# Kernel optimization log

Hardware: AMD Instinct MI355X
Metric: run time of the kernel (lower is better)

The kernel has to match this reference:

```python
import jax, jax.numpy as jnp
import numpy as np

N, D = 16384, 2048

def setup_inputs() -> dict:
    key = jax.random.key(0)
    k1, k2 = jax.random.split(key)
    F = jax.random.normal(k1, (N, D), dtype=jnp.float32)
    F_star = jax.random.normal(k2, (N, D), dtype=jnp.float32)
    lambda_r = jnp.float32(1.0)
    return {"F": F, "F_star": F_star, "lambda_r": lambda_r}

def reference(F, F_star, lambda_r):
    # trace(F F^T Fs Fs^T) == ||F^T Fs||_F^2 (cyclic trace property);
    # avoids materializing the n x n Gram matrices the torch code forms.
    G = jnp.einsum('nd,ne->de', F, F_star)  # [D, D]
    return lambda_r * jnp.sum(G * G)
```

## Files before the change

kernel.cpp:

```cpp
#include <hip/hip_runtime.h>
#include <hip/hip_bf16.h>

#define N_ROWS 16384
#define D_DIM  2048
#define SPLITK 4
#define NS     (N_ROWS / 32)
#define NP     (D_DIM / 128)


typedef __attribute__((ext_vector_type(8))) short short8;
typedef __attribute__((ext_vector_type(4))) float f32x4;
typedef __attribute__((ext_vector_type(8))) unsigned short ushort8;
typedef __attribute__((ext_vector_type(4))) unsigned short ushort4v;

#define GPTR(p) ((const __attribute__((address_space(1))) void*)(p))
#define LPTR(p) ((__attribute__((address_space(3))) void*)(p))

__device__ __forceinline__ unsigned short f2bf(float x) {
  __hip_bfloat16 b = __float2bfloat16(x);
  return *reinterpret_cast<unsigned short*>(&b);
}
__device__ __forceinline__ float bf2f(unsigned short u) {
  unsigned int v = ((unsigned int)u) << 16;
  return *reinterpret_cast<float*>(&v);
}

__global__ void __launch_bounds__(256) transpose_pack(
    const float* __restrict__ F, const float* __restrict__ Fs,
    unsigned short* __restrict__ Fb, unsigned short* __restrict__ Fsb) {
  const float* src = blockIdx.z ? Fs : F;
  unsigned short* dst = blockIdx.z ? Fsb : Fb;
  const int t = threadIdx.x;
  const int mt = blockIdx.y;
  const int m0 = mt * 128;
  const int kb0 = blockIdx.x * 64;

  const int mg   = t & 31;
  const int koct = (t >> 5) & 3;
  const int c    = t >> 7;
  const int krow = kb0 + c * 32 + koct * 8;

  float4 r[8];
#pragma unroll
  for (int j = 0; j < 8; ++j)
    r[j] = *(const float4*)&src[(size_t)(krow + j) * D_DIM + m0 + mg * 4];
  const float* rp = (const float*)r;

  const int ks = blockIdx.x * 2 + c;
  unsigned short* base = dst + ((size_t)mt * NS + ks) * 4096
                       + (size_t)(mg >> 2) * 512 + (size_t)koct * 128
                       + (size_t)(mg & 3) * 32;
#pragma unroll
  for (int i = 0; i < 4; ++i) {
    ushort8 o;
#pragma unroll
    for (int j = 0; j < 8; ++j) o[j] = f2bf(rp[j * 4 + i]);
    *(ushort8*)&base[i * 8] = o;
  }
}

__global__ void __launch_bounds__(256) gemm_packed(
    const unsigned short* __restrict__ Fb, const unsigned short* __restrict__ Fsb,
    unsigned short* __restrict__ Cpart) {
  __shared__ unsigned short lds[16384];
  const int tid = threadIdx.x;
  const int wave = tid >> 6, lane = tid & 63;
  const int wm = wave >> 1, wn = wave & 1;
  const int z = blockIdx.z;
  const int NSs = NS / SPLITK;
  const int NIT = NSs / 2;

  size_t offA = ((size_t)blockIdx.y * NS + (size_t)z * NSs) * 4096
              + (size_t)(2 * wave) * 512 + lane * 8;
  size_t offB = ((size_t)blockIdx.x * NS + (size_t)z * NSs) * 4096
              + (size_t)(2 * wave) * 512 + lane * 8;
  unsigned short* lA = &lds[(2 * wave) * 512];
  unsigned short* lB = &lds[8192 + (2 * wave) * 512];

  f32x4 acc[4][4];
#pragma unroll
  for (int i = 0; i < 4; ++i)
#pragma unroll
    for (int j = 0; j < 4; ++j) acc[i][j] = 0.f;

  for (int it = 0; it < NIT; ++it) {
    __builtin_amdgcn_global_load_lds(GPTR(Fb + offA),              LPTR(lA),              16, 0, 0);
    __builtin_amdgcn_global_load_lds(GPTR(Fb + offA + 512),        LPTR(lA + 512),        16, 0, 0);
    __builtin_amdgcn_global_load_lds(GPTR(Fb + offA + 4096),       LPTR(lA + 4096),       16, 0, 0);
    __builtin_amdgcn_global_load_lds(GPTR(Fb + offA + 4096 + 512), LPTR(lA + 4096 + 512), 16, 0, 0);
    __builtin_amdgcn_global_load_lds(GPTR(Fsb + offB),              LPTR(lB),              16, 0, 0);
    __builtin_amdgcn_global_load_lds(GPTR(Fsb + offB + 512),        LPTR(lB + 512),        16, 0, 0);
    __builtin_amdgcn_global_load_lds(GPTR(Fsb + offB + 4096),       LPTR(lB + 4096),       16, 0, 0);
    __builtin_amdgcn_global_load_lds(GPTR(Fsb + offB + 4096 + 512), LPTR(lB + 4096 + 512), 16, 0, 0);
    offA += 8192; offB += 8192;
    __syncthreads();

#pragma unroll
    for (int s = 0; s < 2; ++s) {
      short8 a[4], b[4];
#pragma unroll
      for (int i = 0; i < 4; ++i)
        a[i] = *(const short8*)&lds[s * 4096 + (wm * 4 + i) * 512 + lane * 8];
#pragma unroll
      for (int j = 0; j < 4; ++j)
        b[j] = *(const short8*)&lds[8192 + s * 4096 + (wn * 4 + j) * 512 + lane * 8];
#pragma unroll
      for (int i = 0; i < 4; ++i)
#pragma unroll
        for (int j = 0; j < 4; ++j)
          acc[i][j] = __builtin_amdgcn_mfma_f32_16x16x32_bf16(a[i], b[j], acc[i][j], 0, 0, 0);
    }
    __syncthreads();
  }

  unsigned short* cp = Cpart + (size_t)z * (D_DIM * D_DIM)
                     + (size_t)(blockIdx.y * 16 + blockIdx.x) * 16384 + wave * 4096;
#pragma unroll
  for (int i = 0; i < 4; ++i)
#pragma unroll
    for (int j = 0; j < 4; ++j) {
      ushort4v o;
#pragma unroll
      for (int r = 0; r < 4; ++r) o[r] = f2bf(acc[i][j][r]);
      *(ushort4v*)&cp[(i * 4 + j) * 256 + lane * 4] = o;
    }
}

__global__ void __launch_bounds__(256) reduce_squares(
    const unsigned short* __restrict__ Cpart, const float* __restrict__ lam,
    float* __restrict__ out) {
  const int NQ = (D_DIM * D_DIM) / 8;
  const ushort8* c = (const ushort8*)Cpart;
  float s = 0.f;
  for (int idx = blockIdx.x * 256 + threadIdx.x; idx < NQ; idx += gridDim.x * 256) {
    float v[8];
#pragma unroll
    for (int j = 0; j < 8; ++j) v[j] = 0.f;
#pragma unroll
    for (int z = 0; z < SPLITK; ++z) {
      ushort8 u = c[(size_t)z * NQ + idx];
#pragma unroll
      for (int j = 0; j < 8; ++j) v[j] += bf2f(u[j]);
    }
#pragma unroll
    for (int j = 0; j < 8; ++j) s += v[j] * v[j];
  }
  for (int off = 32; off > 0; off >>= 1) s += __shfl_down(s, off, 64);
  __shared__ float red[4];
  const int wave = threadIdx.x >> 6, lane = threadIdx.x & 63;
  if (lane == 0) red[wave] = s;
  __syncthreads();
  if (threadIdx.x == 0) atomicAdd(out, (red[0] + red[1] + red[2] + red[3]) * lam[0]);
}

__global__ void __launch_bounds__(256) fallback_kernel(
    const float* __restrict__ F, const float* __restrict__ Fs,
    const float* __restrict__ lam, float* __restrict__ out) {
  __shared__ float sA[64][16], sB[64][16];
  const int d0 = blockIdx.y * 16, e0 = blockIdx.x * 16;
  const int t = threadIdx.x;
  const int td = t >> 4, te = t & 15;
  float s = 0.f;
  for (int k0 = 0; k0 < N_ROWS; k0 += 64) {
#pragma unroll
    for (int p = 0; p < 4; ++p) {
      const int k = (t >> 4) + p * 16;
      const int cc = t & 15;
      sA[k][cc] = F[(size_t)(k0 + k) * D_DIM + d0 + cc];
      sB[k][cc] = Fs[(size_t)(k0 + k) * D_DIM + e0 + cc];
    }
    __syncthreads();
#pragma unroll
    for (int kk = 0; kk < 64; ++kk) s += sA[kk][td] * sB[kk][te];
    __syncthreads();
  }
  float q = s * s;
  for (int off = 32; off > 0; off >>= 1) q += __shfl_down(q, off, 64);
  __shared__ float red[4];
  if ((t & 63) == 0) red[t >> 6] = q;
  __syncthreads();
  if (t == 0) atomicAdd(out, (red[0] + red[1] + red[2] + red[3]) * lam[0]);
}

extern "C" void kernel_launch(void* const* d_in, const int* in_sizes, int n_in,
                              void* d_out, int out_size, void* d_ws, size_t ws_size,
                              hipStream_t stream) {
  const float* F   = (const float*)d_in[0];
  const float* Fs  = (const float*)d_in[1];
  const float* lam = (const float*)d_in[2];
  float* out = (float*)d_out;
  hipMemsetAsync(d_out, 0, sizeof(float) * (size_t)out_size, stream);

  const size_t bf_bytes = (size_t)NP * NS * 8192;
  const size_t cpart_bytes = (size_t)SPLITK * D_DIM * D_DIM * 2;
  const size_t need = 2 * bf_bytes + cpart_bytes;

  if (ws_size >= need) {
    unsigned short* Fb  = (unsigned short*)d_ws;
    unsigned short* Fsb = Fb + bf_bytes / 2;
    unsigned short* Cpart = (unsigned short*)((char*)d_ws + 2 * bf_bytes);
    transpose_pack<<<dim3(N_ROWS / 64, NP, 2), 256, 0, stream>>>(F, Fs, Fb, Fsb);
    gemm_packed<<<dim3(16, 16, SPLITK), 256, 0, stream>>>(Fb, Fsb, Cpart);
    reduce_squares<<<dim3(1024), 256, 0, stream>>>(Cpart, lam, out);
  } else {
    fallback_kernel<<<dim3(128, 128), 256, 0, stream>>>(F, Fs, lam, out);
  }
}
```

Measured before the change: 499.4 us.

## Rework GEMM into 256x256 tiles with 8 waves and double-buffered phased LDS pipeline

The packed bf16 GEMM moves from 128x128 tiles with 4 waves to 256x256 tiles with 8 waves and 128KB of LDS. Global-to-LDS loads are double-buffered and interleaved across four MFMA phases, with explicit waitcnt, barriers and setprio. This increases data reuse per tile and is meant to hide memory latency behind matrix math. The risks are lower occupancy, fewer blocks (256 total) and hand-managed synchronization that could be fragile.

Result: faster. 429.7 us (-14.0%).

```diff
diff --git a/kernel.cpp b/kernel.cpp
--- a/kernel.cpp
+++ b/kernel.cpp
@@ -6,6 +6,8 @@
 #define SPLITK 4
 #define NS     (N_ROWS / 32)
 #define NP     (D_DIM / 128)
+#define NSS    (NS / SPLITK)
+#define NKT    (NSS / 2)
 
 
 typedef __attribute__((ext_vector_type(8))) short short8;
@@ -59,71 +61,138 @@
   }
 }
 
-__global__ void __launch_bounds__(256) gemm_packed(
+__global__ void __launch_bounds__(512, 2) gemm_packed(
     const unsigned short* __restrict__ Fb, const unsigned short* __restrict__ Fsb,
     unsigned short* __restrict__ Cpart) {
-  __shared__ unsigned short lds[16384];
+  __shared__ unsigned short lds[65536];
   const int tid = threadIdx.x;
-  const int wave = tid >> 6, lane = tid & 63;
-  const int wm = wave >> 1, wn = wave & 1;
-  const int z = blockIdx.z;
-  const int NSs = NS / SPLITK;
-  const int NIT = NSs / 2;
-
-  size_t offA = ((size_t)blockIdx.y * NS + (size_t)z * NSs) * 4096
-              + (size_t)(2 * wave) * 512 + lane * 8;
-  size_t offB = ((size_t)blockIdx.x * NS + (size_t)z * NSs) * 4096
-              + (size_t)(2 * wave) * 512 + lane * 8;
-  unsigned short* lA = &lds[(2 * wave) * 512];
-  unsigned short* lB = &lds[8192 + (2 * wave) * 512];
-
-  f32x4 acc[4][4];
-#pragma unroll
-  for (int i = 0; i < 4; ++i)
+  const int w = tid >> 6, lane = tid & 63;
+  const int wm = w >> 2, wn = w & 3;
+  const int bx = blockIdx.x, by = blockIdx.y, z = blockIdx.z;
+
+  const size_t kbase = (size_t)z * NSS * 4096;
+  size_t aSrc0 = ((size_t)(by * 2 + 0) * NS) * 4096 + kbase + (size_t)w * 1024 + lane * 8;
+  size_t aSrc1 = ((size_t)(by * 2 + 1) * NS) * 4096 + kbase + (size_t)w * 1024 + lane * 8;
+  size_t bSrc0 = ((size_t)(bx * 2 + 0) * NS) * 4096 + kbase + (size_t)w * 1024 + lane * 8;
+  size_t bSrc1 = ((size_t)(bx * 2 + 1) * NS) * 4096 + kbase + (size_t)w * 1024 + lane * 8;
+
+  const int aRd = wm * 8192 + lane * 8;
+  const int bRd = (wn >> 1) * 8192 + (wn & 1) * 2048 + lane * 8;
+
+#define STAGE_A(KT, P, BUF) do {                                               \
+    int _kt = (KT); if (_kt >= NKT) _kt -= NKT;                                \
+    const unsigned short* _s = Fb + (P ? aSrc1 : aSrc0) + (size_t)_kt * 8192;  \
+    unsigned short* _d = &lds[(BUF) * 16384 + (P) * 8192 + w * 1024];          \
+    __builtin_amdgcn_global_load_lds(GPTR(_s),       LPTR(_d),       16, 0, 0);\
+    __builtin_amdgcn_global_load_lds(GPTR(_s + 512), LPTR(_d + 512), 16, 0, 0);\
+  } while (0)
+#define STAGE_B(KT, Q, BUF) do {                                               \
+    int _kt = (KT); if (_kt >= NKT) _kt -= NKT;                                \
+    const unsigned short* _s = Fsb + (Q ? bSrc1 : bSrc0) + (size_t)_kt * 8192; \
+    unsigned short* _d = &lds[32768 + (BUF) * 16384 + (Q) * 8192 + w * 1024];  \
+    __builtin_amdgcn_global_load_lds(GPTR(_s),       LPTR(_d),       16, 0, 0);\
+    __builtin_amdgcn_global_load_lds(GPTR(_s + 512), LPTR(_d + 512), 16, 0, 0);\
+  } while (0)
+#define LDA(DST, BUF, I, SL) (DST) = *(const short8*)&lds[(BUF) * 16384 + aRd + (SL) * 4096 + (I) * 512]
+#define LDB(DST, BUF, J, SL) (DST) = *(const short8*)&lds[32768 + (BUF) * 16384 + bRd + (SL) * 4096 + (J) * 512]
+
+  f32x4 acc[8][4];
+#pragma unroll
+  for (int i = 0; i < 8; ++i)
 #pragma unroll
     for (int j = 0; j < 4; ++j) acc[i][j] = 0.f;
 
-  for (int it = 0; it < NIT; ++it) {
-    __builtin_amdgcn_global_load_lds(GPTR(Fb + offA),              LPTR(lA),              16, 0, 0);
-    __builtin_amdgcn_global_load_lds(GPTR(Fb + offA + 512),        LPTR(lA + 512),        16, 0, 0);
-    __builtin_amdgcn_global_load_lds(GPTR(Fb + offA + 4096),       LPTR(lA + 4096),       16, 0, 0);
-    __builtin_amdgcn_global_load_lds(GPTR(Fb + offA + 4096 + 512), LPTR(lA + 4096 + 512), 16, 0, 0);
-    __builtin_amdgcn_global_load_lds(GPTR(Fsb + offB),              LPTR(lB),              16, 0, 0);
-    __builtin_amdgcn_global_load_lds(GPTR(Fsb + offB + 512),        LPTR(lB + 512),        16, 0, 0);
-    __builtin_amdgcn_global_load_lds(GPTR(Fsb + offB + 4096),       LPTR(lB + 4096),       16, 0, 0);
-    __builtin_amdgcn_global_load_lds(GPTR(Fsb + offB + 4096 + 512), LPTR(lB + 4096 + 512), 16, 0, 0);
-    offA += 8192; offB += 8192;
-    __syncthreads();
-
-#pragma unroll
-    for (int s = 0; s < 2; ++s) {
-      short8 a[4], b[4];
-#pragma unroll
-      for (int i = 0; i < 4; ++i)
-        a[i] = *(const short8*)&lds[s * 4096 + (wm * 4 + i) * 512 + lane * 8];
-#pragma unroll
-      for (int j = 0; j < 4; ++j)
-        b[j] = *(const short8*)&lds[8192 + s * 4096 + (wn * 4 + j) * 512 + lane * 8];
-#pragma unroll
-      for (int i = 0; i < 4; ++i)
-#pragma unroll
-        for (int j = 0; j < 4; ++j)
-          acc[i][j] = __builtin_amdgcn_mfma_f32_16x16x32_bf16(a[i], b[j], acc[i][j], 0, 0, 0);
-    }
-    __syncthreads();
+  short8 aR[4][2], bLo[2][2], bHi[2][2];
+
+  STAGE_A(0, 0, 0); STAGE_A(0, 1, 0);
+  STAGE_B(0, 0, 0); STAGE_B(0, 1, 0);
+  STAGE_B(1, 0, 1); STAGE_B(1, 1, 1);
+  asm volatile("s_waitcnt vmcnt(4)" ::: "memory");
+  __builtin_amdgcn_s_barrier();
+
+#define PHASE1(T, B) do {                                                      \
+    _Pragma("unroll") for (int i = 0; i < 4; ++i) {                            \
+      LDA(aR[i][0], B, i, 0); LDA(aR[i][1], B, i, 1); }                        \
+    _Pragma("unroll") for (int j = 0; j < 2; ++j) {                            \
+      LDB(bLo[j][0], B, j, 0); LDB(bLo[j][1], B, j, 1); }                      \
+    STAGE_A((T) + 1, 0, (B) ^ 1);                                              \
+    asm volatile("s_waitcnt lgkmcnt(8)" ::: "memory");                         \
+    __builtin_amdgcn_s_barrier();                                              \
+    asm volatile("s_waitcnt lgkmcnt(0)" ::: "memory");                         \
+    __builtin_amdgcn_s_setprio(1);                                             \
+    _Pragma("unroll") for (int sl = 0; sl < 2; ++sl)                           \
+      _Pragma("unroll") for (int i = 0; i < 4; ++i)                            \
+        _Pragma("unroll") for (int j = 0; j < 2; ++j)                          \
+          acc[i][j] = __builtin_amdgcn_mfma_f32_16x16x32_bf16(aR[i][sl], bLo[j][sl], acc[i][j], 0, 0, 0); \
+    __builtin_amdgcn_s_setprio(0);                                             \
+    __builtin_amdgcn_s_barrier();                                              \
+  } while (0)
+#define PHASE2(T, B) do {                                                      \
+    _Pragma("unroll") for (int j = 0; j < 2; ++j) {                            \
+      LDB(bHi[j][0], B, 2 + j, 0); LDB(bHi[j][1], B, 2 + j, 1); }              \
+    STAGE_A((T) + 1, 1, (B) ^ 1);                                              \
+    __builtin_amdgcn_s_barrier();                                              \
+    asm volatile("s_waitcnt lgkmcnt(0)" ::: "memory");                         \
+    __builtin_amdgcn_s_setprio(1);                                             \
+    _Pragma("unroll") for (int sl = 0; sl < 2; ++sl)                           \
+      _Pragma("unroll") for (int i = 0; i < 4; ++i)                            \
+        _Pragma("unroll") for (int j = 0; j < 2; ++j)                          \
+          acc[i][2 + j] = __builtin_amdgcn_mfma_f32_16x16x32_bf16(aR[i][sl], bHi[j][sl], acc[i][2 + j], 0, 0, 0); \
+    __builtin_amdgcn_s_setprio(0);                                             \
+    __builtin_amdgcn_s_barrier();                                              \
+  } while (0)
+#define PHASE3(T, B) do {                                                      \
+    _Pragma("unroll") for (int i = 0; i < 4; ++i) {                            \
+      LDA(aR[i][0], B, 4 + i, 0); LDA(aR[i][1], B, 4 + i, 1); }                \
+    STAGE_B((T) + 2, 0, B);                                                    \
+    __builtin_amdgcn_s_barrier();                                              \
+    asm volatile("s_waitcnt lgkmcnt(0)" ::: "memory");                         \
+    __builtin_amdgcn_s_setprio(1);                                             \
+    _Pragma("unroll") for (int sl = 0; sl < 2; ++sl)                           \
+      _Pragma("unroll") for (int i = 0; i < 4; ++i)                            \
+        _Pragma("unroll") for (int j = 0; j < 2; ++j)                          \
+          acc[4 + i][2 + j] = __builtin_amdgcn_mfma_f32_16x16x32_bf16(aR[i][sl], bHi[j][sl], acc[4 + i][2 + j], 0, 0, 0); \
+    __builtin_amdgcn_s_setprio(0);                                             \
+    __builtin_amdgcn_s_barrier();                                              \
+  } while (0)
+#define PHASE4(T, B) do {                                                      \
+    STAGE_B((T) + 2, 1, B);                                                    \
+    __builtin_amdgcn_s_barrier();                                              \
+    asm volatile("s_waitcnt lgkmcnt(0)" ::: "memory");                         \
+    __builtin_amdgcn_s_setprio(1);                                             \
+    _Pragma("unroll") for (int sl = 0; sl < 2; ++sl)                           \
+      _Pragma("unroll") for (int i = 0; i < 4; ++i)                            \
+        _Pragma("unroll") for (int j = 0; j < 2; ++j)                          \
+          acc[4 + i][j] = __builtin_amdgcn_mfma_f32_16x16x32_bf16(aR[i][sl], bLo[j][sl], acc[4 + i][j], 0, 0, 0); \
+    __builtin_amdgcn_s_setprio(0);                                             \
+    asm volatile("s_waitcnt vmcnt(4)" ::: "memory");                           \
+    __builtin_amdgcn_s_barrier();                                              \
+  } while (0)
+
+  for (int t = 0; t < NKT; t += 2) {
+    PHASE1(t, 0); PHASE2(t, 0); PHASE3(t, 0); PHASE4(t, 0);
+    PHASE1(t + 1, 1); PHASE2(t + 1, 1); PHASE3(t + 1, 1); PHASE4(t + 1, 1);
   }
 
   unsigned short* cp = Cpart + (size_t)z * (D_DIM * D_DIM)
-                     + (size_t)(blockIdx.y * 16 + blockIdx.x) * 16384 + wave * 4096;
-#pragma unroll
-  for (int i = 0; i < 4; ++i)
+                     + (size_t)(by * 8 + bx) * 65536 + w * 8192 + lane * 4;
+#pragma unroll
+  for (int i = 0; i < 8; ++i)
 #pragma unroll
     for (int j = 0; j < 4; ++j) {
       ushort4v o;
 #pragma unroll
       for (int r = 0; r < 4; ++r) o[r] = f2bf(acc[i][j][r]);
-      *(ushort4v*)&cp[(i * 4 + j) * 256 + lane * 4] = o;
+      *(ushort4v*)&cp[(i * 4 + j) * 256] = o;
     }
+#undef STAGE_A
+#undef STAGE_B
+#undef LDA
+#undef LDB
+#undef PHASE1
+#undef PHASE2
+#undef PHASE3
+#undef PHASE4
 }
 
 __global__ void __launch_bounds__(256) reduce_squares(
@@ -200,7 +269,7 @@
     unsigned short* Fsb = Fb + bf_bytes / 2;
     unsigned short* Cpart = (unsigned short*)((char*)d_ws + 2 * bf_bytes);
     transpose_pack<<<dim3(N_ROWS / 64, NP, 2), 256, 0, stream>>>(F, Fs, Fb, Fsb);
-    gemm_packed<<<dim3(16, 16, SPLITK), 256, 0, stream>>>(Fb, Fsb, Cpart);
+    gemm_packed<<<dim3(8, 8, SPLITK), 512, 0, stream>>>(Fb, Fsb, Cpart);
     reduce_squares<<<dim3(1024), 256, 0, stream>>>(Cpart, lam, out);
   } else {
     fallback_kernel<<<dim3(128, 128), 256, 0, stream>>>(F, Fs, lam, out);
```
